# Optimization experiments

Measured on AMD Instinct MI355X. Metric: run time of the kernel, lower is better.

Reference implementation:

```python
import jax, jax.numpy as jnp
import numpy as np

E = 1024      # embed_dim
QH = 16       # query heads
KVH = 4       # kv heads
HD = E // QH  # head_dim = 64
KVE = HD * KVH  # 256
EPS = 1e-5
ROPE_BASE = 10000.0


def rope(x, d):
    # Faithful to the source RoPE: d == number of heads (x.shape[-2]),
    # and the 'sequence' axis of the cache is x.shape[0] (the batch dim).
    # rope(x) = x*cos + (x*sin) * neg_half(x)  (note: nonlinear in x).
    b = x.shape[0]
    theta = 1.0 / (ROPE_BASE ** (jnp.arange(0, d, 2, dtype=jnp.float32) / d))  # (d//2,)
    seq_idx = jnp.arange(b, dtype=jnp.float32)                                 # (b,)
    idx_theta = seq_idx[:, None] * theta[None, :]                              # (b, d//2)
    idx2 = jnp.concatenate([idx_theta, idx_theta], axis=-1)                    # (b, d)
    # cached shape (b,1,1,d); source permutes (0,1,3,2) -> (b,1,d,1)
    cos = jnp.cos(idx2)[:, None, :, None]  # (b,1,d,1)
    sin = jnp.sin(idx2)[:, None, :, None]
    d2 = d // 2
    # split of the LAST dim (head_dim) at d//2 == num_heads//2, as in source
    neg = jnp.concatenate([-x[..., d2:], x[..., :d2]], axis=-1)
    return x * cos + (x * sin) * neg


def setup_inputs() -> dict:
    key = jax.random.key(0)
    ks = jax.random.split(key, 12)
    b, n = 1, 2048

    def xavier(k, shape):
        fan_out, fan_in = shape
        std = (2.0 / (fan_in + fan_out)) ** 0.5
        return jax.random.normal(k, shape, dtype=jnp.float32) * std

    return {
        "query": jax.random.normal(ks[0], (b, n, E), dtype=jnp.float32),
        "key": jax.random.normal(ks[1], (b, n, E), dtype=jnp.float32),
        "value": jax.random.normal(ks[2], (b, n, E), dtype=jnp.float32),
        "Wq": xavier(ks[3], (E, E)),
        "bq": jnp.zeros((E,), jnp.float32),
        "Wk": xavier(ks[4], (KVE, E)),
        "bk": jnp.zeros((KVE,), jnp.float32),
        "Wv": xavier(ks[5], (KVE, E)),
        "bv": jnp.zeros((KVE,), jnp.float32),
        "gamma": jnp.ones((E,), jnp.float32),
        "beta": jnp.zeros((E,), jnp.float32),
    }


def reference(query, key, value, Wq, bq, Wk, bk, Wv, bv, gamma, beta):
    b, n, _ = query.shape
    q = query @ Wq.T + bq            # (b,n,E)
    k = key @ Wk.T + bk              # (b,n,KVE)
    v = value @ Wv.T + bv            # (b,n,KVE)

    q = q.reshape(b, n, QH, HD)      # b n h d
    k = k.reshape(b, n, KVH, HD)
    v = v.reshape(b, n, KVH, HD)

    q = rope(q, QH)
    k = rope(k, KVH)

    # b n h d -> b h n d
    q = jnp.transpose(q, (0, 2, 1, 3))
    k = jnp.transpose(k, (0, 2, 1, 3))
    v = jnp.transpose(v, (0, 2, 1, 3))

    scale = float(HD) ** 0.5
    q = q / scale

    g = QH // KVH
    # 'b (h g) n d -> b g h n d' : h outer, g inner
    q = q.reshape(b, KVH, g, n, HD)              # (b, h, g, n, d)
    q = jnp.transpose(q, (0, 2, 1, 3, 4))        # (b, g, h, n, d)

    sim = jnp.einsum('bghnd,bhsd->bghns', q, k)  # (b,g,h,n,s)
    attn = jax.nn.softmax(sim, axis=-1)
    out = jnp.einsum('bghns,bhsd->bghnd', attn, v)

    # 'b g h n d -> b n (h g) d'
    out = jnp.transpose(out, (0, 3, 2, 1, 4))    # (b, n, h, g, d)
    x = out.reshape(b, n, QH * HD)               # (b, n, E)

    # LayerNorm (biased variance, as in torch)
    mu = jnp.mean(x, axis=-1, keepdims=True)
    var = jnp.mean((x - mu) ** 2, axis=-1, keepdims=True)
    x = (x - mu) * jax.lax.rsqrt(var + EPS) * gamma + beta

    # NOTE: source computes out_proj(x) but returns x, so out_proj is dead code.
    return x
```

## Files before the change

kernel.cpp:

```cpp
#include <hip/hip_runtime.h>
#include <math.h>

#define EDIM   1024
#define KVEDIM 256
#define HDIM   64
#define QHEADS 16

typedef __attribute__((ext_vector_type(8))) short short8;
typedef __attribute__((ext_vector_type(4))) float f32x4;

__device__ __forceinline__ unsigned pack2(float a, float b) {
    unsigned ua = __builtin_bit_cast(unsigned, a);
    unsigned ub = __builtin_bit_cast(unsigned, b);
    ua += 0x7fffu + ((ua >> 16) & 1u);
    ub += 0x7fffu + ((ub >> 16) & 1u);
    return (ua >> 16) | (ub & 0xffff0000u);
}
__device__ __forceinline__ short f2b(float a) {
    unsigned ua = __builtin_bit_cast(unsigned, a);
    ua += 0x7fffu + ((ua >> 16) & 1u);
    return (short)(ua >> 16);
}

__global__ __launch_bounds__(256)
void proj_gemm(const float* __restrict__ Aq, const float* __restrict__ Ak,
               const float* __restrict__ Av,
               const float* __restrict__ Wq, const float* __restrict__ Wk,
               const float* __restrict__ Wv,
               const float* __restrict__ bq, const float* __restrict__ bk,
               const float* __restrict__ bv,
               short* __restrict__ Cq, short* __restrict__ Ck,
               short* __restrict__ Cv, float qscale)
{
    const int z = blockIdx.z;
    const float* A; const float* W; const float* bias; short* C; int N; float scale;
    if (z == 0)      { A = Aq; W = Wq; bias = bq; C = Cq; N = EDIM;   scale = qscale; }
    else if (z == 1) { A = Ak; W = Wk; bias = bk; C = Ck; N = KVEDIM; scale = 1.0f; }
    else             { A = Av; W = Wv; bias = bv; C = Cv; N = KVEDIM; scale = 1.0f; }
    if ((int)blockIdx.x * 128 >= N) return;
    const int K = EDIM;

    __shared__ short As[64 * 72];
    __shared__ short Ws[128 * 72];

    const int t    = threadIdx.x;
    const int lane = t & 63, wave = t >> 6;
    const int lm   = lane & 15;
    const int q8   = (lane >> 4) * 8;
    const int wm   = (wave >> 1) * 32, wn = (wave & 1) * 64;
    const int bm   = blockIdx.y * 64,  bn = blockIdx.x * 128;

    const int sr = t >> 4;
    const int sc = (t & 15) * 4;

    f32x4 zero = {0.f, 0.f, 0.f, 0.f};
    f32x4 acc[2][4];
    #pragma unroll
    for (int i = 0; i < 2; ++i)
        #pragma unroll
        for (int j = 0; j < 4; ++j) acc[i][j] = zero;

    for (int k0 = 0; k0 < K; k0 += 64) {
        __syncthreads();
        #pragma unroll
        for (int i = 0; i < 4; ++i) {
            int r = sr + i * 16;
            float4 av = *(const float4*)&A[(size_t)(bm + r) * K + k0 + sc];
            uint2 p; p.x = pack2(av.x, av.y); p.y = pack2(av.z, av.w);
            *(uint2*)&As[r * 72 + sc] = p;
        }
        #pragma unroll
        for (int i = 0; i < 8; ++i) {
            int r = sr + i * 16;
            float4 wv = *(const float4*)&W[(size_t)(bn + r) * K + k0 + sc];
            uint2 p; p.x = pack2(wv.x, wv.y); p.y = pack2(wv.z, wv.w);
            *(uint2*)&Ws[r * 72 + sc] = p;
        }
        __syncthreads();
        #pragma unroll
        for (int ks = 0; ks < 2; ++ks) {
            short8 af[2], bfr[4];
            #pragma unroll
            for (int i = 0; i < 2; ++i)
                af[i] = *(const short8*)&As[(wm + i * 16 + lm) * 72 + ks * 32 + q8];
            #pragma unroll
            for (int j = 0; j < 4; ++j)
                bfr[j] = *(const short8*)&Ws[(wn + j * 16 + lm) * 72 + ks * 32 + q8];
            #pragma unroll
            for (int i = 0; i < 2; ++i)
                #pragma unroll
                for (int j = 0; j < 4; ++j)
                    acc[i][j] = __builtin_amdgcn_mfma_f32_16x16x32_bf16(
                        af[i], bfr[j], acc[i][j], 0, 0, 0);
        }
    }

    const int q4 = (lane >> 4) * 4;
    #pragma unroll
    for (int j = 0; j < 4; ++j) {
        float bj = bias[bn + wn + j * 16 + lm];
        #pragma unroll
        for (int i = 0; i < 2; ++i)
            #pragma unroll
            for (int r = 0; r < 4; ++r) {
                int row = bm + wm + i * 16 + q4 + r;
                C[(size_t)row * N + bn + wn + j * 16 + lm] =
                    f2b((acc[i][j][r] + bj) * scale);
            }
    }
}

__global__ __launch_bounds__(256)
void attn_mfma(const short* __restrict__ q, const short* __restrict__ k,
               const short* __restrict__ v, float* __restrict__ x, int n)
{
    __shared__ short Ks[64 * 72];
    __shared__ short Vt[64 * 72];
    __shared__ short Ps[64 * 72];

    const int qh = blockIdx.y, kvh = qh >> 2;
    const int r0 = blockIdx.x * 64;
    const int t  = threadIdx.x;
    const int lane = t & 63, wave = t >> 6;
    const int lm = lane & 15;
    const int q8 = (lane >> 4) * 8, q4 = (lane >> 4) * 4;

    const short* qrow = &q[(size_t)(r0 + wave * 16 + lm) * EDIM + qh * HDIM];
    short8 qf0 = *(const short8*)&qrow[q8];
    short8 qf1 = *(const short8*)&qrow[32 + q8];

    f32x4 zero = {0.f, 0.f, 0.f, 0.f};
    f32x4 oacc[4];
    #pragma unroll
    for (int dt = 0; dt < 4; ++dt) oacc[dt] = zero;
    float l_i[4] = {0.f, 0.f, 0.f, 0.f};

    const int krow = t >> 2, kc = (t & 3) * 8;
    const int vs4 = (t & 15) * 4, vd0 = (t >> 4) * 4;

    for (int s0 = 0; s0 < n; s0 += 64) {
        __syncthreads();
        {
            const uint4* ksrc = (const uint4*)&k[(size_t)(s0 + krow) * KVEDIM + kvh * HDIM];
            uint4 ka = ksrc[t & 3];
            uint4 kb = ksrc[(t & 3) + 4];
            *(uint4*)&Ks[krow * 72 + kc] = ka;
            *(uint4*)&Ks[krow * 72 + kc + 32] = kb;
        }
        {
            unsigned vr[4][2];
            #pragma unroll
            for (int i = 0; i < 4; ++i) {
                uint2 vv = *(const uint2*)&v[(size_t)(s0 + vs4 + i) * KVEDIM + kvh * HDIM + vd0];
                vr[i][0] = vv.x; vr[i][1] = vv.y;
            }
            #pragma unroll
            for (int j = 0; j < 4; ++j) {
                int w = j >> 1, hi = (j & 1) * 16;
                unsigned e0 = (vr[0][w] >> hi) & 0xffffu;
                unsigned e1 = (vr[1][w] >> hi) & 0xffffu;
                unsigned e2 = (vr[2][w] >> hi) & 0xffffu;
                unsigned e3 = (vr[3][w] >> hi) & 0xffffu;
                uint2 o; o.x = e0 | (e1 << 16); o.y = e2 | (e3 << 16);
                *(uint2*)&Vt[(vd0 + j) * 72 + vs4] = o;
            }
        }
        __syncthreads();

        f32x4 sacc[4];
        #pragma unroll
        for (int nt = 0; nt < 4; ++nt) {
            short8 kf0 = *(const short8*)&Ks[(nt * 16 + lm) * 72 + q8];
            short8 kf1 = *(const short8*)&Ks[(nt * 16 + lm) * 72 + 32 + q8];
            f32x4 zz = zero;
            zz = __builtin_amdgcn_mfma_f32_16x16x32_bf16(qf0, kf0, zz, 0, 0, 0);
            sacc[nt] = __builtin_amdgcn_mfma_f32_16x16x32_bf16(qf1, kf1, zz, 0, 0, 0);
        }

        #pragma unroll
        for (int nt = 0; nt < 4; ++nt)
            #pragma unroll
            for (int r = 0; r < 4; ++r) {
                float p = exp2f(sacc[nt][r]);
                l_i[r] += p;
                Ps[(wave * 16 + q4 + r) * 72 + nt * 16 + lm] = f2b(p);
            }

        #pragma unroll
        for (int ks = 0; ks < 2; ++ks) {
            short8 pf = *(const short8*)&Ps[(wave * 16 + lm) * 72 + ks * 32 + q8];
            #pragma unroll
            for (int dt = 0; dt < 4; ++dt) {
                short8 vf = *(const short8*)&Vt[(dt * 16 + lm) * 72 + ks * 32 + q8];
                oacc[dt] = __builtin_amdgcn_mfma_f32_16x16x32_bf16(pf, vf, oacc[dt], 0, 0, 0);
            }
        }
    }

    float inv[4];
    #pragma unroll
    for (int r = 0; r < 4; ++r) {
        float l = l_i[r];
        l += __shfl_xor(l, 1);
        l += __shfl_xor(l, 2);
        l += __shfl_xor(l, 4);
        l += __shfl_xor(l, 8);
        inv[r] = 1.0f / l;
    }
    #pragma unroll
    for (int dt = 0; dt < 4; ++dt)
        #pragma unroll
        for (int r = 0; r < 4; ++r)
            x[(size_t)(r0 + wave * 16 + q4 + r) * EDIM + qh * HDIM + dt * 16 + lm] =
                oacc[dt][r] * inv[r];
}

__global__ __launch_bounds__(256)
void ln_kernel(float* __restrict__ x, const float* __restrict__ gamma,
               const float* __restrict__ beta)
{
    const int rowbase = (int)blockIdx.x * EDIM;
    const int t = threadIdx.x;

    float4 xv = *(const float4*)&x[rowbase + t * 4];
    float s  = xv.x + xv.y + xv.z + xv.w;
    float sq = xv.x * xv.x + xv.y * xv.y + xv.z * xv.z + xv.w * xv.w;
    #pragma unroll
    for (int m = 1; m < 64; m <<= 1) {
        s  += __shfl_xor(s,  m);
        sq += __shfl_xor(sq, m);
    }
    __shared__ float ws_[4], wq_[4];
    const int wave = t >> 6;
    if ((t & 63) == 0) { ws_[wave] = s; wq_[wave] = sq; }
    __syncthreads();
    s  = ws_[0] + ws_[1] + ws_[2] + ws_[3];
    sq = wq_[0] + wq_[1] + wq_[2] + wq_[3];

    const float mu   = s * (1.f / EDIM);
    const float var  = sq * (1.f / EDIM) - mu * mu;
    const float rstd = rsqrtf(var + 1e-5f);

    float4 g = *(const float4*)&gamma[t * 4];
    float4 b = *(const float4*)&beta[t * 4];
    float4 o;
    o.x = (xv.x - mu) * rstd * g.x + b.x;
    o.y = (xv.y - mu) * rstd * g.y + b.y;
    o.z = (xv.z - mu) * rstd * g.z + b.z;
    o.w = (xv.w - mu) * rstd * g.w + b.w;
    *(float4*)&x[rowbase + t * 4] = o;
}

extern "C" void kernel_launch(void* const* d_in, const int* in_sizes, int n_in,
                              void* d_out, int out_size, void* d_ws, size_t ws_size,
                              hipStream_t stream)
{
    const float* query = (const float*)d_in[0];
    const float* key   = (const float*)d_in[1];
    const float* value = (const float*)d_in[2];
    const float* Wq    = (const float*)d_in[3];
    const float* bq    = (const float*)d_in[4];
    const float* Wk    = (const float*)d_in[5];
    const float* bk    = (const float*)d_in[6];
    const float* Wv    = (const float*)d_in[7];
    const float* bv    = (const float*)d_in[8];
    const float* gamma = (const float*)d_in[9];
    const float* beta  = (const float*)d_in[10];
    float* out = (float*)d_out;

    const int n = in_sizes[0] / EDIM;

    short* qb = (short*)d_ws;
    short* kb = qb + (size_t)n * EDIM;
    short* vb = kb + (size_t)n * KVEDIM;

    const float qscale = 0.125f * 1.44269504088896f;

    proj_gemm<<<dim3(EDIM / 128, n / 64, 3), 256, 0, stream>>>(
        query, key, value, Wq, Wk, Wv, bq, bk, bv, qb, kb, vb, qscale);
    attn_mfma<<<dim3(n / 64, QHEADS), 256, 0, stream>>>(qb, kb, vb, out, n);
    ln_kernel<<<dim3(n), 256, 0, stream>>>(out, gamma, beta);
}
```

Measured before the change: 185.9 us.

## Pre-convert inputs to bf16, enlarge GEMM tiles, restructure attention wave split

Adds a separate kernel that converts all activations and weights to bf16 up front, so the projection GEMM loads bf16 directly and no longer re-converts fp32 tiles on every pass. The GEMM moves to 128x128 tiles on a flat 192-block grid, removing the wasted blocks of the old z-indexed launch and increasing reuse per load. Attention now has each wave compute scores for its own 16 keys against all 64 queries, then the waves split the PV product across rows and head-dim tiles, with row sums reduced through shared memory. The cost is an extra launch and a full fp32-read, bf16-write pass over the inputs, one more barrier per key tile, and fewer GEMM blocks than the GPU has CUs.

```diff
diff --git a/kernel.cpp b/kernel.cpp
--- a/kernel.cpp
+++ b/kernel.cpp
@@ -23,40 +23,73 @@
 }
 
 __global__ __launch_bounds__(256)
-void proj_gemm(const float* __restrict__ Aq, const float* __restrict__ Ak,
-               const float* __restrict__ Av,
-               const float* __restrict__ Wq, const float* __restrict__ Wk,
-               const float* __restrict__ Wv,
+void cvt_bf16(const float* __restrict__ s0, const float* __restrict__ s1,
+              const float* __restrict__ s2, const float* __restrict__ s3,
+              const float* __restrict__ s4, const float* __restrict__ s5,
+              short* __restrict__ d0, short* __restrict__ d1,
+              short* __restrict__ d2, short* __restrict__ d3,
+              short* __restrict__ d4, short* __restrict__ d5,
+              int n0, int n1, int n2, int n3, int n4, int n5)
+{
+    const float* s; short* d; int n;
+    switch (blockIdx.y) {
+        case 0: s = s0; d = d0; n = n0; break;
+        case 1: s = s1; d = d1; n = n1; break;
+        case 2: s = s2; d = d2; n = n2; break;
+        case 3: s = s3; d = d3; n = n3; break;
+        case 4: s = s4; d = d4; n = n4; break;
+        default: s = s5; d = d5; n = n5; break;
+    }
+    int i = ((int)blockIdx.x * 256 + threadIdx.x) * 8;
+    if (i >= n) return;
+    float4 a = *(const float4*)&s[i];
+    float4 b = *(const float4*)&s[i + 4];
+    uint4 o;
+    o.x = pack2(a.x, a.y); o.y = pack2(a.z, a.w);
+    o.z = pack2(b.x, b.y); o.w = pack2(b.z, b.w);
+    *(uint4*)&d[i] = o;
+}
+
+__global__ __launch_bounds__(256)
+void proj_gemm(const short* __restrict__ Aq, const short* __restrict__ Ak,
+               const short* __restrict__ Av,
+               const short* __restrict__ Wqb, const short* __restrict__ Wkb,
+               const short* __restrict__ Wvb,
                const float* __restrict__ bq, const float* __restrict__ bk,
                const float* __restrict__ bv,
                short* __restrict__ Cq, short* __restrict__ Ck,
                short* __restrict__ Cv, float qscale)
 {
-    const int z = blockIdx.z;
-    const float* A; const float* W; const float* bias; short* C; int N; float scale;
-    if (z == 0)      { A = Aq; W = Wq; bias = bq; C = Cq; N = EDIM;   scale = qscale; }
-    else if (z == 1) { A = Ak; W = Wk; bias = bk; C = Ck; N = KVEDIM; scale = 1.0f; }
-    else             { A = Av; W = Wv; bias = bv; C = Cv; N = KVEDIM; scale = 1.0f; }
-    if ((int)blockIdx.x * 128 >= N) return;
+    const int bid = blockIdx.x;
+    const short* A; const short* W; const float* bias; short* C;
+    int N, bm, bn; float scale;
+    if (bid < 128) {
+        A = Aq; W = Wqb; bias = bq; C = Cq; N = EDIM; scale = qscale;
+        bm = (bid >> 3) * 128; bn = (bid & 7) * 128;
+    } else if (bid < 160) {
+        int i = bid - 128;
+        A = Ak; W = Wkb; bias = bk; C = Ck; N = KVEDIM; scale = 1.0f;
+        bm = (i >> 1) * 128; bn = (i & 1) * 128;
+    } else {
+        int i = bid - 160;
+        A = Av; W = Wvb; bias = bv; C = Cv; N = KVEDIM; scale = 1.0f;
+        bm = (i >> 1) * 128; bn = (i & 1) * 128;
+    }
     const int K = EDIM;
 
-    __shared__ short As[64 * 72];
+    __shared__ short As[128 * 72];
     __shared__ short Ws[128 * 72];
 
-    const int t    = threadIdx.x;
-    const int lane = t & 63, wave = t >> 6;
-    const int lm   = lane & 15;
-    const int q8   = (lane >> 4) * 8;
-    const int wm   = (wave >> 1) * 32, wn = (wave & 1) * 64;
-    const int bm   = blockIdx.y * 64,  bn = blockIdx.x * 128;
-
-    const int sr = t >> 4;
-    const int sc = (t & 15) * 4;
+    const int t = threadIdx.x, lane = t & 63, wv = t >> 6;
+    const int lm = lane & 15, quad = lane >> 4;
+    const int q8 = quad * 8, q4 = quad * 4;
+    const int wm = (wv & 1) * 64, wn = (wv >> 1) * 64;
+    const int sr = t >> 3, sc = (t & 7) * 8;
 
     f32x4 zero = {0.f, 0.f, 0.f, 0.f};
-    f32x4 acc[2][4];
-    #pragma unroll
-    for (int i = 0; i < 2; ++i)
+    f32x4 acc[4][4];
+    #pragma unroll
+    for (int i = 0; i < 4; ++i)
         #pragma unroll
         for (int j = 0; j < 4; ++j) acc[i][j] = zero;
 
@@ -64,30 +97,22 @@
         __syncthreads();
         #pragma unroll
         for (int i = 0; i < 4; ++i) {
-            int r = sr + i * 16;
-            float4 av = *(const float4*)&A[(size_t)(bm + r) * K + k0 + sc];
-            uint2 p; p.x = pack2(av.x, av.y); p.y = pack2(av.z, av.w);
-            *(uint2*)&As[r * 72 + sc] = p;
-        }
-        #pragma unroll
-        for (int i = 0; i < 8; ++i) {
-            int r = sr + i * 16;
-            float4 wv = *(const float4*)&W[(size_t)(bn + r) * K + k0 + sc];
-            uint2 p; p.x = pack2(wv.x, wv.y); p.y = pack2(wv.z, wv.w);
-            *(uint2*)&Ws[r * 72 + sc] = p;
+            int r = sr + i * 32;
+            *(uint4*)&As[r * 72 + sc] = *(const uint4*)&A[(size_t)(bm + r) * K + k0 + sc];
+            *(uint4*)&Ws[r * 72 + sc] = *(const uint4*)&W[(size_t)(bn + r) * K + k0 + sc];
         }
         __syncthreads();
         #pragma unroll
         for (int ks = 0; ks < 2; ++ks) {
-            short8 af[2], bfr[4];
-            #pragma unroll
-            for (int i = 0; i < 2; ++i)
+            short8 af[4], bfr[4];
+            #pragma unroll
+            for (int i = 0; i < 4; ++i)
                 af[i] = *(const short8*)&As[(wm + i * 16 + lm) * 72 + ks * 32 + q8];
             #pragma unroll
             for (int j = 0; j < 4; ++j)
                 bfr[j] = *(const short8*)&Ws[(wn + j * 16 + lm) * 72 + ks * 32 + q8];
             #pragma unroll
-            for (int i = 0; i < 2; ++i)
+            for (int i = 0; i < 4; ++i)
                 #pragma unroll
                 for (int j = 0; j < 4; ++j)
                     acc[i][j] = __builtin_amdgcn_mfma_f32_16x16x32_bf16(
@@ -95,18 +120,15 @@
         }
     }
 
-    const int q4 = (lane >> 4) * 4;
     #pragma unroll
     for (int j = 0; j < 4; ++j) {
         float bj = bias[bn + wn + j * 16 + lm];
         #pragma unroll
-        for (int i = 0; i < 2; ++i)
-            #pragma unroll
-            for (int r = 0; r < 4; ++r) {
-                int row = bm + wm + i * 16 + q4 + r;
-                C[(size_t)row * N + bn + wn + j * 16 + lm] =
+        for (int i = 0; i < 4; ++i)
+            #pragma unroll
+            for (int r = 0; r < 4; ++r)
+                C[(size_t)(bm + wm + i * 16 + q4 + r) * N + bn + wn + j * 16 + lm] =
                     f2b((acc[i][j][r] + bj) * scale);
-            }
     }
 }
 
@@ -117,23 +139,33 @@
     __shared__ short Ks[64 * 72];
     __shared__ short Vt[64 * 72];
     __shared__ short Ps[64 * 72];
+    __shared__ float Lred[4][64];
 
     const int qh = blockIdx.y, kvh = qh >> 2;
     const int r0 = blockIdx.x * 64;
-    const int t  = threadIdx.x;
-    const int lane = t & 63, wave = t >> 6;
-    const int lm = lane & 15;
-    const int q8 = (lane >> 4) * 8, q4 = (lane >> 4) * 4;
-
-    const short* qrow = &q[(size_t)(r0 + wave * 16 + lm) * EDIM + qh * HDIM];
-    short8 qf0 = *(const short8*)&qrow[q8];
-    short8 qf1 = *(const short8*)&qrow[32 + q8];
+    const int t = threadIdx.x;
+    const int lane = t & 63, wv = t >> 6;
+    const int lm = lane & 15, quad = lane >> 4;
+    const int q8 = quad * 8, q4 = quad * 4;
+
+    short8 qf[4][2];
+    #pragma unroll
+    for (int qt = 0; qt < 4; ++qt) {
+        const short* qrow = &q[(size_t)(r0 + qt * 16 + lm) * EDIM + qh * HDIM];
+        qf[qt][0] = *(const short8*)&qrow[q8];
+        qf[qt][1] = *(const short8*)&qrow[32 + q8];
+    }
+
+    const int rt0 = (wv & 1) * 2;
+    const int dt0 = (wv >> 1) * 2;
 
     f32x4 zero = {0.f, 0.f, 0.f, 0.f};
-    f32x4 oacc[4];
-    #pragma unroll
-    for (int dt = 0; dt < 4; ++dt) oacc[dt] = zero;
-    float l_i[4] = {0.f, 0.f, 0.f, 0.f};
+    f32x4 oacc[2][2];
+    #pragma unroll
+    for (int i = 0; i < 2; ++i)
+        #pragma unroll
+        for (int j = 0; j < 2; ++j) oacc[i][j] = zero;
+    float lp[4] = {0.f, 0.f, 0.f, 0.f};
 
     const int krow = t >> 2, kc = (t & 3) * 8;
     const int vs4 = (t & 15) * 4, vd0 = (t >> 4) * 4;
@@ -167,52 +199,63 @@
         }
         __syncthreads();
 
-        f32x4 sacc[4];
-        #pragma unroll
-        for (int nt = 0; nt < 4; ++nt) {
-            short8 kf0 = *(const short8*)&Ks[(nt * 16 + lm) * 72 + q8];
-            short8 kf1 = *(const short8*)&Ks[(nt * 16 + lm) * 72 + 32 + q8];
-            f32x4 zz = zero;
-            zz = __builtin_amdgcn_mfma_f32_16x16x32_bf16(qf0, kf0, zz, 0, 0, 0);
-            sacc[nt] = __builtin_amdgcn_mfma_f32_16x16x32_bf16(qf1, kf1, zz, 0, 0, 0);
-        }
-
-        #pragma unroll
-        for (int nt = 0; nt < 4; ++nt)
-            #pragma unroll
-            for (int r = 0; r < 4; ++r) {
-                float p = exp2f(sacc[nt][r]);
-                l_i[r] += p;
-                Ps[(wave * 16 + q4 + r) * 72 + nt * 16 + lm] = f2b(p);
+        short8 kf0 = *(const short8*)&Ks[(wv * 16 + lm) * 72 + q8];
+        short8 kf1 = *(const short8*)&Ks[(wv * 16 + lm) * 72 + 32 + q8];
+        #pragma unroll
+        for (int qt = 0; qt < 4; ++qt) {
+            f32x4 s = zero;
+            s = __builtin_amdgcn_mfma_f32_16x16x32_bf16(kf0, qf[qt][0], s, 0, 0, 0);
+            s = __builtin_amdgcn_mfma_f32_16x16x32_bf16(kf1, qf[qt][1], s, 0, 0, 0);
+            float p0 = exp2f(s[0]);
+            float p1 = exp2f(s[1]);
+            float p2 = exp2f(s[2]);
+            float p3 = exp2f(s[3]);
+            lp[qt] += (p0 + p1) + (p2 + p3);
+            uint2 pw; pw.x = pack2(p0, p1); pw.y = pack2(p2, p3);
+            *(uint2*)&Ps[(qt * 16 + lm) * 72 + wv * 16 + q4] = pw;
+        }
+        __syncthreads();
+
+        short8 vf[2][2];
+        #pragma unroll
+        for (int j = 0; j < 2; ++j) {
+            vf[j][0] = *(const short8*)&Vt[((dt0 + j) * 16 + lm) * 72 + q8];
+            vf[j][1] = *(const short8*)&Vt[((dt0 + j) * 16 + lm) * 72 + 32 + q8];
+        }
+        #pragma unroll
+        for (int i = 0; i < 2; ++i) {
+            short8 pf0 = *(const short8*)&Ps[((rt0 + i) * 16 + lm) * 72 + q8];
+            short8 pf1 = *(const short8*)&Ps[((rt0 + i) * 16 + lm) * 72 + 32 + q8];
+            #pragma unroll
+            for (int j = 0; j < 2; ++j) {
+                oacc[i][j] = __builtin_amdgcn_mfma_f32_16x16x32_bf16(pf0, vf[j][0], oacc[i][j], 0, 0, 0);
+                oacc[i][j] = __builtin_amdgcn_mfma_f32_16x16x32_bf16(pf1, vf[j][1], oacc[i][j], 0, 0, 0);
             }
-
-        #pragma unroll
-        for (int ks = 0; ks < 2; ++ks) {
-            short8 pf = *(const short8*)&Ps[(wave * 16 + lm) * 72 + ks * 32 + q8];
-            #pragma unroll
-            for (int dt = 0; dt < 4; ++dt) {
-                short8 vf = *(const short8*)&Vt[(dt * 16 + lm) * 72 + ks * 32 + q8];
-                oacc[dt] = __builtin_amdgcn_mfma_f32_16x16x32_bf16(pf, vf, oacc[dt], 0, 0, 0);
-            }
-        }
-    }
-
-    float inv[4];
-    #pragma unroll
-    for (int r = 0; r < 4; ++r) {
-        float l = l_i[r];
-        l += __shfl_xor(l, 1);
-        l += __shfl_xor(l, 2);
-        l += __shfl_xor(l, 4);
-        l += __shfl_xor(l, 8);
-        inv[r] = 1.0f / l;
-    }
-    #pragma unroll
-    for (int dt = 0; dt < 4; ++dt)
-        #pragma unroll
-        for (int r = 0; r < 4; ++r)
-            x[(size_t)(r0 + wave * 16 + q4 + r) * EDIM + qh * HDIM + dt * 16 + lm] =
-                oacc[dt][r] * inv[r];
+        }
+    }
+
+    #pragma unroll
+    for (int qt = 0; qt < 4; ++qt) {
+        float l = lp[qt];
+        l += __shfl_xor(l, 16);
+        l += __shfl_xor(l, 32);
+        if (lane < 16) Lred[wv][qt * 16 + lm] = l;
+    }
+    __syncthreads();
+
+    #pragma unroll
+    for (int i = 0; i < 2; ++i) {
+        #pragma unroll
+        for (int r = 0; r < 4; ++r) {
+            int row = (rt0 + i) * 16 + q4 + r;
+            float lsum = (Lred[0][row] + Lred[1][row]) + (Lred[2][row] + Lred[3][row]);
+            float inv = 1.0f / lsum;
+            #pragma unroll
+            for (int j = 0; j < 2; ++j)
+                x[(size_t)(r0 + row) * EDIM + qh * HDIM + (dt0 + j) * 16 + lm] =
+                    oacc[i][j][r] * inv;
+        }
+    }
 }
 
 __global__ __launch_bounds__(256)
@@ -270,14 +313,27 @@
 
     const int n = in_sizes[0] / EDIM;
 
-    short* qb = (short*)d_ws;
-    short* kb = qb + (size_t)n * EDIM;
-    short* vb = kb + (size_t)n * KVEDIM;
+    short* qa  = (short*)d_ws;
+    short* ka  = qa  + (size_t)n * EDIM;
+    short* va  = ka  + (size_t)n * EDIM;
+    short* wqb = va  + (size_t)n * EDIM;
+    short* wkb = wqb + (size_t)EDIM * EDIM;
+    short* wvb = wkb + (size_t)KVEDIM * EDIM;
+    short* qb  = wvb + (size_t)KVEDIM * EDIM;
+    short* kb  = qb  + (size_t)n * EDIM;
+    short* vb  = kb  + (size_t)n * KVEDIM;
 
     const float qscale = 0.125f * 1.44269504088896f;
 
-    proj_gemm<<<dim3(EDIM / 128, n / 64, 3), 256, 0, stream>>>(
-        query, key, value, Wq, Wk, Wv, bq, bk, bv, qb, kb, vb, qscale);
+    cvt_bf16<<<dim3(1024, 6), 256, 0, stream>>>(
+        query, key, value, Wq, Wk, Wv,
+        qa, ka, va, wqb, wkb, wvb,
+        n * EDIM, n * EDIM, n * EDIM, EDIM * EDIM, KVEDIM * EDIM, KVEDIM * EDIM);
+
+    proj_gemm<<<dim3(192), 256, 0, stream>>>(
+        qa, ka, va, wqb, wkb, wvb, bq, bk, bv, qb, kb, vb, qscale);
+
     attn_mfma<<<dim3(n / 64, QHEADS), 256, 0, stream>>>(qb, kb, vb, out, n);
+
     ln_kernel<<<dim3(n), 256, 0, stream>>>(out, gamma, beta);
 }
```

Result: faster. 176.1 us (-5.3%).
